# Kernel optimization log

Measured on AMD Instinct MI355X. Metric: run time of the kernel, lower is better.

Reference implementation:

```python
import jax, jax.numpy as jnp
import numpy as np

B, H, S, D = 2, 16, 4096, 64
NUM_GLOBAL = 64  # number of global tokens (first NUM_GLOBAL positions)


def setup_inputs() -> dict:
    key = jax.random.key(0)
    k1, k2, k3 = jax.random.split(key, 3)
    q = jax.random.normal(k1, (B, H, S, D), dtype=jnp.float32)
    k = jax.random.normal(k2, (B, H, S, D), dtype=jnp.float32)
    v = jax.random.normal(k3, (B, H, S, D), dtype=jnp.float32)
    attention_mask = jnp.zeros((B, S), dtype=jnp.int32).at[:, :NUM_GLOBAL].set(1)
    return {"q": q, "k": k, "v": v, "attention_mask": attention_mask,
            "max_global": NUM_GLOBAL}


def reference(q, k, v, attention_mask, max_global):
    b, h, s, d = q.shape
    bh = b * h
    G = int(max_global)  # static, equals is_global.sum(1).max() in torch code
    scale = d ** 0.5

    qf = q.reshape(bh, s, d)
    kf = k.reshape(bh, s, d)
    vf = v.reshape(bh, s, d)

    # is_global expanded over heads: [bh, s]
    is_global = jnp.broadcast_to((attention_mask > 0)[:, None, :], (b, h, s)).reshape(bh, s)
    # slot index within the compacted global-KV cache; invalid -> dump slot G
    pos = jnp.cumsum(is_global.astype(jnp.int32), axis=1) - 1
    pos = jnp.where(is_global, pos, G)                      # [bh, s]
    row = jnp.arange(bh)[:, None]                           # [bh, 1]

    # scatter k/v of global tokens into compact caches (extra dump slot sliced off)
    global_k = jnp.zeros((bh, G + 1, d), qf.dtype).at[row, pos].set(kf)[:, :G]
    global_v = jnp.zeros((bh, G + 1, d), qf.dtype).at[row, pos].set(vf)[:, :G]
    gmask = jnp.zeros((bh, G + 1), bool).at[row, pos].set(True)[:, :G]
    # inverse map: token position of each global slot
    tok = jnp.arange(s, dtype=jnp.int32)[None, :]
    token_pos = jnp.zeros((bh, G + 1), jnp.int32).at[row, pos].set(
        jnp.broadcast_to(tok, (bh, s)))[:, :G]             # [bh, G]

    # every query attends to the global KV cache
    scores = jnp.einsum('bsd,bgd->bsg', qf / scale, global_k)
    scores = jnp.where(gmask[:, None, :], scores, -jnp.inf)
    probs = jax.nn.softmax(scores.astype(jnp.float32), axis=-1)  # [bh, s, G]
    context = jnp.einsum('bsg,bgd->bsd', probs, global_v)

    # global query tokens do full attention over all keys of their batch-head
    qg = jnp.take_along_axis(qf, token_pos[:, :, None], axis=1)   # [bh, G, d]
    scores_g = jnp.einsum('bgd,bsd->bgs', qg, kf) / scale
    probs_g = jax.nn.softmax(scores_g.astype(jnp.float32), axis=-1)
    context_g = jnp.einsum('bgs,bsd->bgd', probs_g, vf)           # [bh, G, d]

    # scatter global contexts back into their token positions (dump row s for invalid)
    dest = jnp.where(gmask, token_pos, s)
    context = jnp.concatenate(
        [context, jnp.zeros((bh, 1, d), context.dtype)], axis=1
    ).at[row, dest].set(context_g)[:, :s]

    return (context.reshape(b, h, s, d), probs.reshape(b, h, s, G))
```

## Files before the change

### kernel.cpp

```cpp
#include <hip/hip_runtime.h>
#include <hip/hip_bf16.h>
#include <cstddef>

constexpr int CB  = 2;
constexpr int CH  = 16;
constexpr int CS  = 4096;
constexpr int CD  = 64;
constexpr int CG  = 64;
constexpr int CBH = CB * CH;
constexpr int NS1 = 8;
constexpr int NS2 = 8;
constexpr int NPART = 16;

#define QSCALE 0.18033688011112042f

typedef float  f32x16 __attribute__((ext_vector_type(16)));
typedef short  short8 __attribute__((ext_vector_type(8)));
typedef float  fvec4  __attribute__((ext_vector_type(4)));

union U8 { unsigned u[4]; short8 s; };

__device__ __forceinline__ unsigned short f2bf(float x) {
  union { __hip_bfloat16 h; unsigned short u; } cv;
  cv.h = __float2bfloat16(x);
  return cv.u;
}
__device__ __forceinline__ unsigned pk2(float lo, float hi) {
  union { __hip_bfloat162 h; unsigned u; } cv;
  cv.h.x = __float2bfloat16(lo);
  cv.h.y = __float2bfloat16(hi);
  return cv.u;
}
__device__ __forceinline__ f32x16 zero16() {
  f32x16 z;
#pragma unroll
  for (int i = 0; i < 16; ++i) z[i] = 0.f;
  return z;
}

#define MK_PA(dst, hi_, a0,a1,a2,a3,a4,a5,a6,a7)                         \
  {                                                                      \
    unsigned x0 = pk2(a0, a1), x1 = pk2(a2, a3);                         \
    unsigned y0 = pk2(a4, a5), y1 = pk2(a6, a7);                         \
    unsigned t0 = (unsigned)__shfl_xor((int)((hi_) ? x0 : y0), 32);      \
    if (hi_) x0 = t0; else y0 = t0;                                      \
    unsigned t1 = (unsigned)__shfl_xor((int)((hi_) ? x1 : y1), 32);      \
    if (hi_) x1 = t1; else y1 = t1;                                      \
    U8 w_; w_.u[0] = x0; w_.u[1] = x1; w_.u[2] = y0; w_.u[3] = y1;       \
    dst = w_.s;                                                          \
  }

struct __align__(16) SMemP1 { short sK[64 * 64]; short sVT[64 * 64]; };
struct __align__(16) SMemP2 { short sK2[2][64 * 64]; short sVT2[2][64 * 64]; };
union __align__(16) SMem { SMemP1 p1; SMemP2 p2; };

__global__ __launch_bounds__(256, 2) void k_main(
    const float* __restrict__ q, const float* __restrict__ k,
    const float* __restrict__ v, const int* __restrict__ mask,
    float* __restrict__ ctx, float* __restrict__ probs,
    float* __restrict__ pm, float* __restrict__ pl,
    unsigned short* __restrict__ pctx,
    int* __restrict__ gpos_ws, int* __restrict__ gcount_ws) {
  __shared__ SMem sm;
  __shared__ int gp[CG];
  __shared__ int gc_s;
  __shared__ int wsum[4];
  const int bh = blockIdx.y, b = bh / CH, t = threadIdx.x;
  const int lane = t & 63, wv = t >> 6;
  const int hi = lane >> 5, ql = lane & 31;
  const unsigned kswz = (unsigned)((ql & 7) << 4);
  const bool isP1 = (blockIdx.x < NS1);

  {
    if (t < CG) gp[t] = 0;
    const int4* mp = (const int4*)(mask + b * CS + t * 16);
    int4 mv[4];
#pragma unroll
    for (int i = 0; i < 4; ++i) mv[i] = mp[i];
    int bits = 0, c = 0;
#pragma unroll
    for (int i = 0; i < 4; ++i) {
      const int4 m4 = mv[i];
      const int b0 = (m4.x > 0), b1 = (m4.y > 0), b2 = (m4.z > 0), b3 = (m4.w > 0);
      bits |= (b0 | (b1 << 1) | (b2 << 2) | (b3 << 3)) << (4 * i);
      c += b0 + b1 + b2 + b3;
    }
    int x = c;
#pragma unroll
    for (int d = 1; d < 64; d <<= 1) {
      const int y = __shfl_up(x, d);
      if (lane >= d) x += y;
    }
    if (lane == 63) wsum[wv] = x;
    __syncthreads();
    int pre = x - c;
    for (int w = 0; w < wv; ++w) pre += wsum[w];
#pragma unroll
    for (int i = 0; i < 16; ++i) {
      if (bits & (1 << i)) {
        if (pre < CG) gp[pre] = t * 16 + i;
        ++pre;
      }
    }
    if (t == 255) gc_s = (pre < CG) ? pre : CG;
    __syncthreads();
  }

  if (isP1) {
    const int bx1 = blockIdx.x;
    const int gc = gc_s;
    if (t < 128) {
      const int row = t >> 1, c0 = (t & 1) * 32;
      const int grow = gp[row];
      const float* src = k + ((size_t)(bh * CS + grow)) * CD + c0;
      fvec4 ra[8];
#pragma unroll
      for (int i = 0; i < 4; ++i) {
        ra[2 * i]     = *(const fvec4*)(src + i * 8);
        ra[2 * i + 1] = *(const fvec4*)(src + i * 8 + 4);
      }
      const unsigned swz = (unsigned)((row & 7) << 4);
      char* rb = (char*)sm.p1.sK + row * 128;
#pragma unroll
      for (int i = 0; i < 4; ++i) {
        U8 w;
        w.u[0] = pk2(ra[2 * i][0], ra[2 * i][1]);
        w.u[1] = pk2(ra[2 * i][2], ra[2 * i][3]);
        w.u[2] = pk2(ra[2 * i + 1][0], ra[2 * i + 1][1]);
        w.u[3] = pk2(ra[2 * i + 1][2], ra[2 * i + 1][3]);
        *(short8*)(rb + (((unsigned)(c0 * 2 + i * 16)) ^ swz)) = w.s;
      }
    } else {
      const int u = t - 128;
      const int kg = u >> 4, cg = u & 15;
      int gi[8];
#pragma unroll
      for (int i = 0; i < 8; ++i) gi[i] = gp[8 * kg + i];
      fvec4 rv[8];
#pragma unroll
      for (int i = 0; i < 8; ++i)
        rv[i] = *(const fvec4*)(v + ((size_t)(bh * CS + gi[i])) * CD + 4 * cg);
#pragma unroll
      for (int c = 0; c < 4; ++c) {
        const int row = 4 * cg + c;
        U8 w;
        w.u[0] = pk2(rv[0][c], rv[1][c]); w.u[1] = pk2(rv[2][c], rv[3][c]);
        w.u[2] = pk2(rv[4][c], rv[5][c]); w.u[3] = pk2(rv[6][c], rv[7][c]);
        *(short8*)((char*)sm.p1.sVT + row * 128 +
                   (((unsigned)(16 * kg)) ^ ((unsigned)((row & 7) << 4)))) = w.s;
      }
    }
    __syncthreads();

#pragma unroll
    for (int it = 0; it < 4; ++it) {
      const int qbase = (bx1 * 4 + it) * 128;
      const int qrow = qbase + wv * 32 + ql;
      const float* qr = q + ((size_t)(bh * CS + qrow)) * CD + hi * 8;
      fvec4 qa[8];
#pragma unroll
      for (int s = 0; s < 4; ++s) {
        qa[2 * s]     = *(const fvec4*)(qr + s * 16);
        qa[2 * s + 1] = *(const fvec4*)(qr + s * 16 + 4);
      }
      short8 qf[4];
#pragma unroll
      for (int s = 0; s < 4; ++s) {
        U8 w;
        w.u[0] = pk2(qa[2 * s][0] * QSCALE, qa[2 * s][1] * QSCALE);
        w.u[1] = pk2(qa[2 * s][2] * QSCALE, qa[2 * s][3] * QSCALE);
        w.u[2] = pk2(qa[2 * s + 1][0] * QSCALE, qa[2 * s + 1][1] * QSCALE);
        w.u[3] = pk2(qa[2 * s + 1][2] * QSCALE, qa[2 * s + 1][3] * QSCALE);
        qf[s] = w.s;
      }

      f32x16 acc0 = zero16(), acc1 = zero16();
#pragma unroll
      for (int s = 0; s < 4; ++s) {
        const unsigned off = ((unsigned)(32 * s + 16 * hi)) ^ kswz;
        short8 k0 = *(const short8*)((char*)sm.p1.sK + ql * 128 + off);
        acc0 = __builtin_amdgcn_mfma_f32_32x32x16_bf16(k0, qf[s], acc0, 0, 0, 0);
        short8 k1 = *(const short8*)((char*)sm.p1.sK + (32 + ql) * 128 + off);
        acc1 = __builtin_amdgcn_mfma_f32_32x32x16_bf16(k1, qf[s], acc1, 0, 0, 0);
      }

      float e0[16], e1[16];
      float m = -1e30f;
#pragma unroll
      for (int r = 0; r < 16; ++r) {
        const int key0 = (r & 3) + 8 * (r >> 2) + 4 * hi;
        float x0 = (key0 < gc) ? acc0[r] : -1e30f;
        float x1 = (key0 + 32 < gc) ? acc1[r] : -1e30f;
        e0[r] = x0; e1[r] = x1;
        m = fmaxf(m, fmaxf(x0, x1));
      }
      m = fmaxf(m, __shfl_xor(m, 32));
      float ls = 0.f;
#pragma unroll
      for (int r = 0; r < 16; ++r) {
        e0[r] = __builtin_exp2f(e0[r] - m); ls += e0[r];
        e1[r] = __builtin_exp2f(e1[r] - m); ls += e1[r];
      }
      ls += __shfl_xor(ls, 32);
      const float inv = 1.0f / ls;
#pragma unroll
      for (int r = 0; r < 16; ++r) { e0[r] *= inv; e1[r] *= inv; }

      float* prow = probs + ((size_t)(bh * CS + qrow)) * CG;
#pragma unroll
      for (int g4 = 0; g4 < 4; ++g4) {
        fvec4 o0 = {e0[4 * g4], e0[4 * g4 + 1], e0[4 * g4 + 2], e0[4 * g4 + 3]};
        fvec4 o1 = {e1[4 * g4], e1[4 * g4 + 1], e1[4 * g4 + 2], e1[4 * g4 + 3]};
        *(fvec4*)(prow + 8 * g4 + 4 * hi) = o0;
        *(fvec4*)(prow + 8 * g4 + 4 * hi + 32) = o1;
      }

      short8 pa0, pa1, pa2, pa3;
      MK_PA(pa0, hi, e0[0], e0[1], e0[2], e0[3], e0[4], e0[5], e0[6], e0[7]);
      MK_PA(pa1, hi, e0[8], e0[9], e0[10], e0[11], e0[12], e0[13], e0[14], e0[15]);
      MK_PA(pa2, hi, e1[0], e1[1], e1[2], e1[3], e1[4], e1[5], e1[6], e1[7]);
      MK_PA(pa3, hi, e1[8], e1[9], e1[10], e1[11], e1[12], e1[13], e1[14], e1[15]);

      f32x16 oc0 = zero16(), oc1 = zero16();
#pragma unroll
      for (int s = 0; s < 4; ++s) {
        const short8 pas = (s == 0) ? pa0 : (s == 1) ? pa1 : (s == 2) ? pa2 : pa3;
        const unsigned off = ((unsigned)(32 * s + 16 * hi)) ^ kswz;
        short8 v0 = *(const short8*)((char*)sm.p1.sVT + ql * 128 + off);
        oc0 = __builtin_amdgcn_mfma_f32_32x32x16_bf16(pas, v0, oc0, 0, 0, 0);
        short8 v1 = *(const short8*)((char*)sm.p1.sVT + (32 + ql) * 128 + off);
        oc1 = __builtin_amdgcn_mfma_f32_32x32x16_bf16(pas, v1, oc1, 0, 0, 0);
      }

      float* cb = ctx + ((size_t)(bh * CS + qbase + wv * 32)) * CD;
#pragma unroll
      for (int r = 0; r < 16; ++r) {
        const int qr2 = (r & 3) + 8 * (r >> 2) + 4 * hi;
        cb[(size_t)qr2 * CD + ql] = oc0[r];
        cb[(size_t)qr2 * CD + 32 + ql] = oc1[r];
      }
    }
  } else {
    const int bx2 = blockIdx.x - NS1;
    const int qt = wv & 1, kh = wv >> 1;
    const int qslot = qt * 32 + ql;

    if (bx2 == 0) {
      if (t < CG) gpos_ws[b * CG + t] = gp[t];
      if (t == 0) gcount_ws[b] = gc_s;
    }

    const int gq = gp[qslot];
    const float* qr = q + ((size_t)(bh * CS + gq)) * CD + hi * 8;
    fvec4 qa[8];
#pragma unroll
    for (int s = 0; s < 4; ++s) {
      qa[2 * s]     = *(const fvec4*)(qr + s * 16);
      qa[2 * s + 1] = *(const fvec4*)(qr + s * 16 + 4);
    }
    short8 qf[4];
#pragma unroll
    for (int s = 0; s < 4; ++s) {
      U8 w;
      w.u[0] = pk2(qa[2 * s][0] * QSCALE, qa[2 * s][1] * QSCALE);
      w.u[1] = pk2(qa[2 * s][2] * QSCALE, qa[2 * s][3] * QSCALE);
      w.u[2] = pk2(qa[2 * s + 1][0] * QSCALE, qa[2 * s + 1][1] * QSCALE);
      w.u[3] = pk2(qa[2 * s + 1][2] * QSCALE, qa[2 * s + 1][3] * QSCALE);
      qf[s] = w.s;
    }

    const int krow = t >> 1, kc0 = (t & 1) * 32;
    const int vu = t - 128, vkg = vu >> 4, vcg = vu & 15;

    fvec4 scur[16], snxt[16];
    {
      const int kwin = (bx2 * 4) * 128;
      if (t < 128) {
#pragma unroll
        for (int h = 0; h < 2; ++h) {
          const float* src =
              k + ((size_t)(bh * CS + kwin + h * 64 + krow)) * CD + kc0;
#pragma unroll
          for (int i = 0; i < 4; ++i) {
            scur[h * 8 + 2 * i]     = *(const fvec4*)(src + i * 8);
            scur[h * 8 + 2 * i + 1] = *(const fvec4*)(src + i * 8 + 4);
          }
        }
      } else {
#pragma unroll
        for (int h = 0; h < 2; ++h)
#pragma unroll
          for (int i = 0; i < 8; ++i)
            scur[h * 8 + i] = *(const fvec4*)(
                v + ((size_t)(bh * CS + kwin + h * 64 + 8 * vkg + i)) * CD +
                4 * vcg);
      }
    }

    float m = -1e30f, l = 0.f;
    f32x16 oc0 = zero16(), oc1 = zero16();

#pragma unroll
    for (int u = 0; u < 4; ++u) {
      if (t < 128) {
        const unsigned swz = (unsigned)((krow & 7) << 4);
#pragma unroll
        for (int h = 0; h < 2; ++h) {
          char* rb = (char*)sm.p2.sK2[h] + krow * 128;
#pragma unroll
          for (int i = 0; i < 4; ++i) {
            U8 w;
            w.u[0] = pk2(scur[h * 8 + 2 * i][0], scur[h * 8 + 2 * i][1]);
            w.u[1] = pk2(scur[h * 8 + 2 * i][2], scur[h * 8 + 2 * i][3]);
            w.u[2] = pk2(scur[h * 8 + 2 * i + 1][0], scur[h * 8 + 2 * i + 1][1]);
            w.u[3] = pk2(scur[h * 8 + 2 * i + 1][2], scur[h * 8 + 2 * i + 1][3]);
            *(short8*)(rb + (((unsigned)(kc0 * 2 + i * 16)) ^ swz)) = w.s;
          }
        }
      } else {
#pragma unroll
        for (int h = 0; h < 2; ++h)
#pragma unroll
          for (int c = 0; c < 4; ++c) {
            const int row = 4 * vcg + c;
            U8 w;
            w.u[0] = pk2(scur[h * 8 + 0][c], scur[h * 8 + 1][c]);
            w.u[1] = pk2(scur[h * 8 + 2][c], scur[h * 8 + 3][c]);
            w.u[2] = pk2(scur[h * 8 + 4][c], scur[h * 8 + 5][c]);
            w.u[3] = pk2(scur[h * 8 + 6][c], scur[h * 8 + 7][c]);
            *(short8*)((char*)sm.p2.sVT2[h] + row * 128 +
                       (((unsigned)(16 * vkg)) ^
                        ((unsigned)((row & 7) << 4)))) = w.s;
          }
      }
      __syncthreads();

      if (u < 3) {
        const int kwin = (bx2 * 4 + u + 1) * 128;
        if (t < 128) {
#pragma unroll
          for (int h = 0; h < 2; ++h) {
            const float* src =
                k + ((size_t)(bh * CS + kwin + h * 64 + krow)) * CD + kc0;
#pragma unroll
            for (int i = 0; i < 4; ++i) {
              snxt[h * 8 + 2 * i]     = *(const fvec4*)(src + i * 8);
              snxt[h * 8 + 2 * i + 1] = *(const fvec4*)(src + i * 8 + 4);
            }
          }
        } else {
#pragma unroll
          for (int h = 0; h < 2; ++h)
#pragma unroll
            for (int i = 0; i < 8; ++i)
              snxt[h * 8 + i] = *(const fvec4*)(
                  v + ((size_t)(bh * CS + kwin + h * 64 + 8 * vkg + i)) * CD +
                  4 * vcg);
        }
      }

      const char* bK = (const char*)sm.p2.sK2[kh];
      const char* bVT = (const char*)sm.p2.sVT2[kh];

      f32x16 acc0 = zero16(), acc1 = zero16();
#pragma unroll
      for (int s = 0; s < 4; ++s) {
        const unsigned off = ((unsigned)(32 * s + 16 * hi)) ^ kswz;
        short8 k0 = *(const short8*)(bK + ql * 128 + off);
        acc0 = __builtin_amdgcn_mfma_f32_32x32x16_bf16(k0, qf[s], acc0, 0, 0, 0);
        short8 k1 = *(const short8*)(bK + (32 + ql) * 128 + off);
        acc1 = __builtin_amdgcn_mfma_f32_32x32x16_bf16(k1, qf[s], acc1, 0, 0, 0);
      }

      float e0[16], e1[16];
      float tm = -1e30f;
#pragma unroll
      for (int r = 0; r < 16; ++r) {
        e0[r] = acc0[r]; e1[r] = acc1[r];
        tm = fmaxf(tm, fmaxf(e0[r], e1[r]));
      }
      tm = fmaxf(tm, __shfl_xor(tm, 32));
      const float mnew = fmaxf(m, tm);
      const float rs = __builtin_exp2f(m - mnew);
      l *= rs;
      float add = 0.f;
#pragma unroll
      for (int r = 0; r < 16; ++r) {
        e0[r] = __builtin_exp2f(e0[r] - mnew); add += e0[r];
        e1[r] = __builtin_exp2f(e1[r] - mnew); add += e1[r];
      }
      add += __shfl_xor(add, 32);
      l += add;
      m = mnew;

      float rsf[16];
#pragma unroll
      for (int r = 0; r < 16; ++r) {
        const int qr2 = (r & 3) + 8 * (r >> 2) + 4 * hi;
        rsf[r] = __shfl(rs, qr2);
      }
#pragma unroll
      for (int r = 0; r < 16; ++r) { oc0[r] *= rsf[r]; oc1[r] *= rsf[r]; }

      short8 pa0, pa1, pa2, pa3;
      MK_PA(pa0, hi, e0[0], e0[1], e0[2], e0[3], e0[4], e0[5], e0[6], e0[7]);
      MK_PA(pa1, hi, e0[8], e0[9], e0[10], e0[11], e0[12], e0[13], e0[14], e0[15]);
      MK_PA(pa2, hi, e1[0], e1[1], e1[2], e1[3], e1[4], e1[5], e1[6], e1[7]);
      MK_PA(pa3, hi, e1[8], e1[9], e1[10], e1[11], e1[12], e1[13], e1[14], e1[15]);

#pragma unroll
      for (int s = 0; s < 4; ++s) {
        const short8 pas = (s == 0) ? pa0 : (s == 1) ? pa1 : (s == 2) ? pa2 : pa3;
        const unsigned off = ((unsigned)(32 * s + 16 * hi)) ^ kswz;
        short8 v0 = *(const short8*)(bVT + ql * 128 + off);
        oc0 = __builtin_amdgcn_mfma_f32_32x32x16_bf16(pas, v0, oc0, 0, 0, 0);
        short8 v1 = *(const short8*)(bVT + (32 + ql) * 128 + off);
        oc1 = __builtin_amdgcn_mfma_f32_32x32x16_bf16(pas, v1, oc1, 0, 0, 0);
      }
      __syncthreads();

      if (u < 3) {
#pragma unroll
        for (int i = 0; i < 16; ++i) scur[i] = snxt[i];
      }
    }

    const int part = bx2 * 2 + kh;
    if (hi == 0) {
      const size_t o = ((size_t)(bh * NPART + part)) * CG + qslot;
      pm[o] = m;
      pl[o] = l;
    }
    unsigned short* po =
        pctx + (((size_t)(bh * NPART + part)) * CG + qt * 32) * CD;
#pragma unroll
    for (int r = 0; r < 16; ++r) {
      const int qr2 = (r & 3) + 8 * (r >> 2) + 4 * hi;
      po[(size_t)qr2 * CD + ql] = f2bf(oc0[r]);
      po[(size_t)qr2 * CD + 32 + ql] = f2bf(oc1[r]);
    }
  }
}

__global__ __launch_bounds__(256) void k_combine(
    const float* __restrict__ pm, const float* __restrict__ pl,
    const unsigned short* __restrict__ pctx,
    const int* __restrict__ gpos, const int* __restrict__ gcount,
    float* __restrict__ ctx) {
  const int g = blockIdx.x;
  const int bh = blockIdx.y;
  const int b = bh / CH;
  if (g >= gcount[b]) return;
  const int t = threadIdx.x;
  const int cg = t >> 6, d = t & 63;
  __shared__ float smax[4];
  __shared__ float sl[4];
  __shared__ float sacc[4][64];

  float lm = -1e30f;
#pragma unroll
  for (int j = 0; j < 4; ++j) {
    const int c = cg * 4 + j;
    lm = fmaxf(lm, pm[((size_t)(bh * NPART + c)) * CG + g]);
  }
  if (d == 0) smax[cg] = lm;
  __syncthreads();
  const float m = fmaxf(fmaxf(smax[0], smax[1]), fmaxf(smax[2], smax[3]));

  float L = 0.f, acc = 0.f;
#pragma unroll
  for (int j = 0; j < 4; ++j) {
    const int c = cg * 4 + j;
    const size_t o = ((size_t)(bh * NPART + c)) * CG + g;
    const float w = __builtin_exp2f(pm[o] - m);
    L = fmaf(w, pl[o], L);
    const float x = __uint_as_float((unsigned)pctx[o * CD + d] << 16);
    acc = fmaf(w, x, acc);
  }
  sacc[cg][d] = acc;
  if (d == 0) sl[cg] = L;
  __syncthreads();
  if (cg == 0) {
    const float A = sacc[0][d] + sacc[1][d] + sacc[2][d] + sacc[3][d];
    const float Lt = sl[0] + sl[1] + sl[2] + sl[3];
    const int tok = gpos[b * CG + g];
    ctx[((size_t)(bh * CS + tok)) * CD + d] = A / Lt;
  }
}

extern "C" void kernel_launch(void* const* d_in, const int* in_sizes, int n_in,
                              void* d_out, int out_size, void* d_ws, size_t ws_size,
                              hipStream_t stream) {
  const float* q = (const float*)d_in[0];
  const float* k = (const float*)d_in[1];
  const float* v = (const float*)d_in[2];
  const int* mask = (const int*)d_in[3];

  float* ctx = (float*)d_out;
  float* probs = ctx + (size_t)CBH * CS * CD;

  char* ws = (char*)d_ws;
  int* gpos = (int*)ws;
  int* gcount = (int*)(ws + 512);
  float* pm = (float*)(ws + 1024);
  float* pl = pm + (size_t)CBH * NPART * CG;
  unsigned short* pctx =
      (unsigned short*)(pl + (size_t)CBH * NPART * CG);

  k_main<<<dim3(NS1 + NS2, CBH), dim3(256), 0, stream>>>(
      q, k, v, mask, ctx, probs, pm, pl, pctx, gpos, gcount);
  k_combine<<<dim3(CG, CBH), dim3(256), 0, stream>>>(
      pm, pl, pctx, gpos, gcount, ctx);
}
```

Before: 40.91 us.

## Fuse combine into main kernel via atomic counter barrier; rebalance block split

Drops the separate combine kernel. The full-attention blocks of each batch-head now bump a global atomic counter, spin until all sibling blocks have written their partials, and then merge the partial softmax results in place. The split between pass-1 and pass-2 blocks also moves from 8/8 to 9/7, with strided window loops replacing the fixed 4-iteration loops. This removes one launch and its dependency gap, but adds a memset and a spin-wait that relies on all sibling blocks being co-resident. It also leaves work imbalanced because 32 windows do not divide evenly by 9 or 7.

```diff
diff --git a/kernel.cpp b/kernel.cpp
--- a/kernel.cpp
+++ b/kernel.cpp
@@ -8,9 +8,10 @@
 constexpr int CD  = 64;
 constexpr int CG  = 64;
 constexpr int CBH = CB * CH;
-constexpr int NS1 = 8;
-constexpr int NS2 = 8;
-constexpr int NPART = 16;
+constexpr int NW  = 32;
+constexpr int NS1 = 9;
+constexpr int NS2 = 7;
+constexpr int NPART = NS2 * 2;
 
 #define QSCALE 0.18033688011112042f
 
@@ -59,12 +60,14 @@
     const float* __restrict__ v, const int* __restrict__ mask,
     float* __restrict__ ctx, float* __restrict__ probs,
     float* __restrict__ pm, float* __restrict__ pl,
-    unsigned short* __restrict__ pctx,
-    int* __restrict__ gpos_ws, int* __restrict__ gcount_ws) {
+    unsigned short* __restrict__ pctx, unsigned* __restrict__ cnt) {
   __shared__ SMem sm;
   __shared__ int gp[CG];
   __shared__ int gc_s;
   __shared__ int wsum[4];
+  __shared__ float cmax[4];
+  __shared__ float cl[4];
+  __shared__ float cacc[4][64];
   const int bh = blockIdx.y, b = bh / CH, t = threadIdx.x;
   const int lane = t & 63, wv = t >> 6;
   const int hi = lane >> 5, ql = lane & 31;
@@ -152,9 +155,8 @@
     }
     __syncthreads();
 
-#pragma unroll
-    for (int it = 0; it < 4; ++it) {
-      const int qbase = (bx1 * 4 + it) * 128;
+    for (int w = bx1; w < NW; w += NS1) {
+      const int qbase = w * 128;
       const int qrow = qbase + wv * 32 + ql;
       const float* qr = q + ((size_t)(bh * CS + qrow)) * CD + hi * 8;
       fvec4 qa[8];
@@ -166,12 +168,12 @@
       short8 qf[4];
 #pragma unroll
       for (int s = 0; s < 4; ++s) {
-        U8 w;
-        w.u[0] = pk2(qa[2 * s][0] * QSCALE, qa[2 * s][1] * QSCALE);
-        w.u[1] = pk2(qa[2 * s][2] * QSCALE, qa[2 * s][3] * QSCALE);
-        w.u[2] = pk2(qa[2 * s + 1][0] * QSCALE, qa[2 * s + 1][1] * QSCALE);
-        w.u[3] = pk2(qa[2 * s + 1][2] * QSCALE, qa[2 * s + 1][3] * QSCALE);
-        qf[s] = w.s;
+        U8 wq;
+        wq.u[0] = pk2(qa[2 * s][0] * QSCALE, qa[2 * s][1] * QSCALE);
+        wq.u[1] = pk2(qa[2 * s][2] * QSCALE, qa[2 * s][3] * QSCALE);
+        wq.u[2] = pk2(qa[2 * s + 1][0] * QSCALE, qa[2 * s + 1][1] * QSCALE);
+        wq.u[3] = pk2(qa[2 * s + 1][2] * QSCALE, qa[2 * s + 1][3] * QSCALE);
+        qf[s] = wq.s;
       }
 
       f32x16 acc0 = zero16(), acc1 = zero16();
@@ -244,11 +246,7 @@
     const int bx2 = blockIdx.x - NS1;
     const int qt = wv & 1, kh = wv >> 1;
     const int qslot = qt * 32 + ql;
-
-    if (bx2 == 0) {
-      if (t < CG) gpos_ws[b * CG + t] = gp[t];
-      if (t == 0) gcount_ws[b] = gc_s;
-    }
+    const int gc = gc_s;
 
     const int gq = gp[qslot];
     const float* qr = q + ((size_t)(bh * CS + gq)) * CD + hi * 8;
@@ -261,12 +259,12 @@
     short8 qf[4];
 #pragma unroll
     for (int s = 0; s < 4; ++s) {
-      U8 w;
-      w.u[0] = pk2(qa[2 * s][0] * QSCALE, qa[2 * s][1] * QSCALE);
-      w.u[1] = pk2(qa[2 * s][2] * QSCALE, qa[2 * s][3] * QSCALE);
-      w.u[2] = pk2(qa[2 * s + 1][0] * QSCALE, qa[2 * s + 1][1] * QSCALE);
-      w.u[3] = pk2(qa[2 * s + 1][2] * QSCALE, qa[2 * s + 1][3] * QSCALE);
-      qf[s] = w.s;
+      U8 wq;
+      wq.u[0] = pk2(qa[2 * s][0] * QSCALE, qa[2 * s][1] * QSCALE);
+      wq.u[1] = pk2(qa[2 * s][2] * QSCALE, qa[2 * s][3] * QSCALE);
+      wq.u[2] = pk2(qa[2 * s + 1][0] * QSCALE, qa[2 * s + 1][1] * QSCALE);
+      wq.u[3] = pk2(qa[2 * s + 1][2] * QSCALE, qa[2 * s + 1][3] * QSCALE);
+      qf[s] = wq.s;
     }
 
     const int krow = t >> 1, kc0 = (t & 1) * 32;
@@ -274,7 +272,7 @@
 
     fvec4 scur[16], snxt[16];
     {
-      const int kwin = (bx2 * 4) * 128;
+      const int kwin = bx2 * 128;
       if (t < 128) {
 #pragma unroll
         for (int h = 0; h < 2; ++h) {
@@ -300,8 +298,7 @@
     float m = -1e30f, l = 0.f;
     f32x16 oc0 = zero16(), oc1 = zero16();
 
-#pragma unroll
-    for (int u = 0; u < 4; ++u) {
+    for (int w = bx2; w < NW; w += NS2) {
       if (t < 128) {
         const unsigned swz = (unsigned)((krow & 7) << 4);
 #pragma unroll
@@ -309,12 +306,12 @@
           char* rb = (char*)sm.p2.sK2[h] + krow * 128;
 #pragma unroll
           for (int i = 0; i < 4; ++i) {
-            U8 w;
-            w.u[0] = pk2(scur[h * 8 + 2 * i][0], scur[h * 8 + 2 * i][1]);
-            w.u[1] = pk2(scur[h * 8 + 2 * i][2], scur[h * 8 + 2 * i][3]);
-            w.u[2] = pk2(scur[h * 8 + 2 * i + 1][0], scur[h * 8 + 2 * i + 1][1]);
-            w.u[3] = pk2(scur[h * 8 + 2 * i + 1][2], scur[h * 8 + 2 * i + 1][3]);
-            *(short8*)(rb + (((unsigned)(kc0 * 2 + i * 16)) ^ swz)) = w.s;
+            U8 ww;
+            ww.u[0] = pk2(scur[h * 8 + 2 * i][0], scur[h * 8 + 2 * i][1]);
+            ww.u[1] = pk2(scur[h * 8 + 2 * i][2], scur[h * 8 + 2 * i][3]);
+            ww.u[2] = pk2(scur[h * 8 + 2 * i + 1][0], scur[h * 8 + 2 * i + 1][1]);
+            ww.u[3] = pk2(scur[h * 8 + 2 * i + 1][2], scur[h * 8 + 2 * i + 1][3]);
+            *(short8*)(rb + (((unsigned)(kc0 * 2 + i * 16)) ^ swz)) = ww.s;
           }
         }
       } else {
@@ -323,20 +320,21 @@
 #pragma unroll
           for (int c = 0; c < 4; ++c) {
             const int row = 4 * vcg + c;
-            U8 w;
-            w.u[0] = pk2(scur[h * 8 + 0][c], scur[h * 8 + 1][c]);
-            w.u[1] = pk2(scur[h * 8 + 2][c], scur[h * 8 + 3][c]);
-            w.u[2] = pk2(scur[h * 8 + 4][c], scur[h * 8 + 5][c]);
-            w.u[3] = pk2(scur[h * 8 + 6][c], scur[h * 8 + 7][c]);
+            U8 ww;
+            ww.u[0] = pk2(scur[h * 8 + 0][c], scur[h * 8 + 1][c]);
+            ww.u[1] = pk2(scur[h * 8 + 2][c], scur[h * 8 + 3][c]);
+            ww.u[2] = pk2(scur[h * 8 + 4][c], scur[h * 8 + 5][c]);
+            ww.u[3] = pk2(scur[h * 8 + 6][c], scur[h * 8 + 7][c]);
             *(short8*)((char*)sm.p2.sVT2[h] + row * 128 +
                        (((unsigned)(16 * vkg)) ^
-                        ((unsigned)((row & 7) << 4)))) = w.s;
+                        ((unsigned)((row & 7) << 4)))) = ww.s;
           }
       }
       __syncthreads();
 
-      if (u < 3) {
-        const int kwin = (bx2 * 4 + u + 1) * 128;
+      const int wn = w + NS2;
+      if (wn < NW) {
+        const int kwin = wn * 128;
         if (t < 128) {
 #pragma unroll
           for (int h = 0; h < 2; ++h) {
@@ -419,7 +417,7 @@
       }
       __syncthreads();
 
-      if (u < 3) {
+      if (wn < NW) {
 #pragma unroll
         for (int i = 0; i < 16; ++i) scur[i] = snxt[i];
       }
@@ -439,52 +437,54 @@
       po[(size_t)qr2 * CD + ql] = f2bf(oc0[r]);
       po[(size_t)qr2 * CD + 32 + ql] = f2bf(oc1[r]);
     }
-  }
-}
-
-__global__ __launch_bounds__(256) void k_combine(
-    const float* __restrict__ pm, const float* __restrict__ pl,
-    const unsigned short* __restrict__ pctx,
-    const int* __restrict__ gpos, const int* __restrict__ gcount,
-    float* __restrict__ ctx) {
-  const int g = blockIdx.x;
-  const int bh = blockIdx.y;
-  const int b = bh / CH;
-  if (g >= gcount[b]) return;
-  const int t = threadIdx.x;
-  const int cg = t >> 6, d = t & 63;
-  __shared__ float smax[4];
-  __shared__ float sl[4];
-  __shared__ float sacc[4][64];
-
-  float lm = -1e30f;
-#pragma unroll
-  for (int j = 0; j < 4; ++j) {
-    const int c = cg * 4 + j;
-    lm = fmaxf(lm, pm[((size_t)(bh * NPART + c)) * CG + g]);
-  }
-  if (d == 0) smax[cg] = lm;
-  __syncthreads();
-  const float m = fmaxf(fmaxf(smax[0], smax[1]), fmaxf(smax[2], smax[3]));
-
-  float L = 0.f, acc = 0.f;
-#pragma unroll
-  for (int j = 0; j < 4; ++j) {
-    const int c = cg * 4 + j;
-    const size_t o = ((size_t)(bh * NPART + c)) * CG + g;
-    const float w = __builtin_exp2f(pm[o] - m);
-    L = fmaf(w, pl[o], L);
-    const float x = __uint_as_float((unsigned)pctx[o * CD + d] << 16);
-    acc = fmaf(w, x, acc);
-  }
-  sacc[cg][d] = acc;
-  if (d == 0) sl[cg] = L;
-  __syncthreads();
-  if (cg == 0) {
-    const float A = sacc[0][d] + sacc[1][d] + sacc[2][d] + sacc[3][d];
-    const float Lt = sl[0] + sl[1] + sl[2] + sl[3];
-    const int tok = gpos[b * CG + g];
-    ctx[((size_t)(bh * CS + tok)) * CD + d] = A / Lt;
+
+    __threadfence();
+    __syncthreads();
+    if (t == 0) {
+      atomicAdd(&cnt[bh], 1u);
+      while (__hip_atomic_load(&cnt[bh], __ATOMIC_ACQUIRE,
+                               __HIP_MEMORY_SCOPE_AGENT) < (unsigned)NS2)
+        __builtin_amdgcn_s_sleep(1);
+    }
+    __syncthreads();
+    __threadfence();
+
+    const int cg2 = t >> 6, d = t & 63;
+    for (int g = bx2; g < gc; g += NS2) {
+      float lm = -1e30f;
+#pragma unroll
+      for (int j = 0; j < 4; ++j) {
+        const int c = cg2 * 4 + j;
+        if (c < NPART)
+          lm = fmaxf(lm, pm[((size_t)(bh * NPART + c)) * CG + g]);
+      }
+      if (d == 0) cmax[cg2] = lm;
+      __syncthreads();
+      const float gm = fmaxf(fmaxf(cmax[0], cmax[1]), fmaxf(cmax[2], cmax[3]));
+
+      float L = 0.f, acc = 0.f;
+#pragma unroll
+      for (int j = 0; j < 4; ++j) {
+        const int c = cg2 * 4 + j;
+        if (c < NPART) {
+          const size_t o = ((size_t)(bh * NPART + c)) * CG + g;
+          const float wgt = __builtin_exp2f(pm[o] - gm);
+          L = fmaf(wgt, pl[o], L);
+          const float x = __uint_as_float((unsigned)pctx[o * CD + d] << 16);
+          acc = fmaf(wgt, x, acc);
+        }
+      }
+      cacc[cg2][d] = acc;
+      if (d == 0) cl[cg2] = L;
+      __syncthreads();
+      if (cg2 == 0) {
+        const float A = cacc[0][d] + cacc[1][d] + cacc[2][d] + cacc[3][d];
+        const float Lt = cl[0] + cl[1] + cl[2] + cl[3];
+        const int tok = gp[g];
+        ctx[((size_t)(bh * CS + tok)) * CD + d] = A / Lt;
+      }
+      __syncthreads();
+    }
   }
 }
 
@@ -500,15 +500,14 @@
   float* probs = ctx + (size_t)CBH * CS * CD;
 
   char* ws = (char*)d_ws;
-  int* gpos = (int*)ws;
-  int* gcount = (int*)(ws + 512);
-  float* pm = (float*)(ws + 1024);
+  float* pm = (float*)ws;
   float* pl = pm + (size_t)CBH * NPART * CG;
   unsigned short* pctx =
       (unsigned short*)(pl + (size_t)CBH * NPART * CG);
-
+  unsigned* cnt =
+      (unsigned*)(pctx + (size_t)CBH * NPART * CG * CD);
+
+  hipMemsetAsync(cnt, 0, CBH * sizeof(unsigned), stream);
   k_main<<<dim3(NS1 + NS2, CBH), dim3(256), 0, stream>>>(
-      q, k, v, mask, ctx, probs, pm, pl, pctx, gpos, gcount);
-  k_combine<<<dim3(CG, CBH), dim3(256), 0, stream>>>(
-      pm, pl, pctx, gpos, gcount, ctx);
+      q, k, v, mask, ctx, probs, pm, pl, pctx, cnt);
 }
```

After: 135.6 us. +231.4%, slower.
